# Optimization experiments

Measured on AMD Instinct MI355X. Metric: run time of the kernel, lower is better.

## Reference

```python
import jax, jax.numpy as jnp
import numpy as np

NEAR_LIDAR = 0.01
FAR_LIDAR = 0.81
BOUND = 1.0
DENSITY_SCALE = 1.0


def setup_inputs() -> dict:
    key = jax.random.key(0)
    ks = jax.random.split(key, 8)
    N = 8192
    H, F, OUT = 32, 16, 2
    return {
        "rays_o": jax.random.normal(ks[0], (1, N, 3), jnp.float32) * 0.1,
        "rays_d": jax.random.normal(ks[1], (1, N, 3), jnp.float32),
        "time": jax.random.uniform(ks[2], (1,), jnp.float32),
        "W1": jax.random.normal(ks[3], (4, H), jnp.float32) * 0.1,
        "b1": jnp.zeros((H,), jnp.float32),
        "Wsig": jax.random.normal(ks[4], (H, 1), jnp.float32) * 0.1,
        "Wfeat": jax.random.normal(ks[5], (H, F), jnp.float32) * 0.1,
        "Wa1": jax.random.normal(ks[6], (3 + 3 + F, H), jnp.float32) * 0.1,
        "ba1": jnp.zeros((H,), jnp.float32),
        "Wa2": jax.random.normal(ks[7], (H, OUT), jnp.float32) * 0.1,
        "num_steps": 512,
    }


def reference(rays_o, rays_d, time, W1, b1, Wsig, Wfeat, Wa1, ba1, Wa2, num_steps):
    prefix = rays_o.shape[:-1]
    ro = rays_o.reshape(-1, 3)
    rd = rays_d.reshape(-1, 3)
    N = ro.shape[0]
    dt = ro.dtype

    nears = jnp.full((N, 1), NEAR_LIDAR, dt)
    fars = jnp.full((N, 1), FAR_LIDAR, dt)
    z = jnp.linspace(0.0, 1.0, num_steps, dtype=dt)[None, :]  # [1,S]
    z_vals = nears + (fars - nears) * z                        # [N,S]
    sample_dist = (fars - nears) / num_steps                   # [N,1]

    # sample points, clamped to aabb [-bound, bound]
    xyzs = ro[:, None, :] + rd[:, None, :] * z_vals[..., None]  # [N,S,3]
    xyzs = jnp.clip(xyzs, -BOUND, BOUND)

    # density stub: MLP on (xyz, t) -> sigma, geo_feat
    t = jnp.broadcast_to(time.reshape(-1)[0].astype(dt), (N, num_steps, 1))
    h = jax.nn.relu(jnp.concatenate([xyzs, t], -1) @ W1 + b1)  # [N,S,H]
    sigma = jax.nn.softplus(h @ Wsig)[..., 0]                  # [N,S]
    feat = h @ Wfeat                                           # [N,S,F]

    deltas = z_vals[..., 1:] - z_vals[..., :-1]
    deltas = jnp.concatenate([deltas, jnp.broadcast_to(sample_dist, (N, 1))], -1)
    alphas = 1.0 - jnp.exp(-deltas * DENSITY_SCALE * sigma)    # [N,S]
    alphas_shifted = jnp.concatenate(
        [jnp.ones_like(alphas[..., :1]), 1.0 - alphas + 1e-15], -1)
    weights = alphas * jnp.cumprod(alphas_shifted, -1)[..., :-1]  # [N,S]

    # attribute stub: MLP on (xyz, dir, geo_feat) -> out_lidar_dim, sigmoid
    dirs = jnp.broadcast_to(rd[:, None, :], xyzs.shape)
    attr = jax.nn.sigmoid(
        jax.nn.relu(jnp.concatenate([xyzs, dirs, feat], -1) @ Wa1 + ba1) @ Wa2)

    weights_sum = weights.sum(-1)
    depth = (weights * z_vals).sum(-1)
    image = (weights[..., None] * attr).sum(-2)

    depth = depth.reshape(*prefix)
    image = image.reshape(*prefix, attr.shape[-1])
    weights_sum = weights_sum.reshape(*prefix)
    return depth, image, weights_sum
```

## Files before the change

kernel.cpp:

```cpp
#include <hip/hip_runtime.h>
#include <math.h>

typedef unsigned short u16;
typedef unsigned int   u32;
typedef unsigned long long u64;

typedef __attribute__((ext_vector_type(8))) short     short8;
typedef __attribute__((ext_vector_type(8))) _Float16  half8;
typedef __attribute__((ext_vector_type(2))) __fp16    fp16x2;
typedef __attribute__((ext_vector_type(4))) float     f32x4;
typedef __attribute__((ext_vector_type(2))) float     f32x2;

__device__ __forceinline__ float bf2f(u16 u){ return __uint_as_float(((u32)u)<<16); }
__device__ __forceinline__ u16 f2bf(float f){ u32 x=__float_as_uint(f); return (u16)((x + 0x7FFFu + ((x>>16)&1u))>>16); }
__device__ __forceinline__ u16 f2h_bits(float x){ union{_Float16 f; u16 u;} c; c.f=(_Float16)x; return c.u; }
__device__ __forceinline__ float h2f(u16 b){ union{u16 u; _Float16 f;} c; c.u=b; return (float)c.f; }
__device__ __forceinline__ u32 pkrtz2(float a, float b){
    union{fp16x2 h; u32 u;} c; c.h = __builtin_amdgcn_cvt_pkrtz(a,b); return c.u;
}
__device__ __forceinline__ u32 pk_relu(float a, float b){
    u32 pk = pkrtz2(a, b), r;
    asm("v_pk_max_f16 %0, %1, 0" : "=v"(r) : "v"(pk));
    return r;
}
__device__ __forceinline__ float clamp1(float x){ return __builtin_amdgcn_fmed3f(x, -1.f, 1.f); }
__device__ __forceinline__ float sigmoidf_fast(float x){ return __builtin_amdgcn_rcpf(1.f + __expf(-x)); }
__device__ __forceinline__ float softplusf_fast(float x){ return (x > 15.f) ? x : __logf(1.f + __expf(x)); }
__device__ __forceinline__ void lds_fence(){ asm volatile("s_waitcnt lgkmcnt(0)" ::: "memory"); }

__device__ __forceinline__ int sniff_is_bf16(const void* rays_d) {
    const u16* p = (const u16*)rays_d;
    int sane = 0;
    #pragma unroll
    for (int k = 0; k < 32; ++k) {
        u16 u = p[2 * k];
        int e = (u >> 7) & 0xFF;
        if (u == 0 || (e >= 96 && e <= 144)) ++sane;
    }
    return sane >= 24;
}
__device__ __forceinline__ float ldin(const void* base, int idx, int isbf) {
    return isbf ? bf2f(((const u16*)base)[idx]) : ((const float*)base)[idx];
}

#define NEARL 0.01f
#define FARL  0.81f

__device__ __forceinline__ int unitof(int k){ return (k>>1) + 16*(k&1); }

__global__ void prep_weights(const void* __restrict__ rays_d,
                             const void* __restrict__ W1,  const void* __restrict__ b1,
                             const void* __restrict__ Wsig,const void* __restrict__ Wfeat,
                             const void* __restrict__ Wa1, const void* __restrict__ ba1,
                             const void* __restrict__ Wa2, u16* __restrict__ wsb)
{
    __shared__ float raw[1504];
    const int tid = threadIdx.x;
    const int isbf = sniff_is_bf16(rays_d);
    for (int i = tid; i < 1504; i += 512) {
        float v;
        if (i < 128)       v = ldin(W1,   i,        isbf);
        else if (i < 160)  v = ldin(b1,   i - 128,  isbf);
        else if (i < 192)  v = ldin(Wsig, i - 160,  isbf);
        else if (i < 704)  v = ldin(Wfeat,i - 192,  isbf);
        else if (i < 1408) v = ldin(Wa1,  i - 704,  isbf);
        else if (i < 1440) v = ldin(ba1,  i - 1408, isbf);
        else               v = ldin(Wa2,  i - 1440, isbf);
        raw[i] = v;
    }
    __syncthreads();
    const float* rW1  = raw;
    const float* rb1  = raw + 128;
    const float* rWs  = raw + 160;
    const float* rWf  = raw + 192;
    const float* rWa1 = raw + 704;
    const float* rba  = raw + 1408;
    const float* rWa2 = raw + 1440;

    const int p = tid >> 6, l = tid & 63;
    const int q = l >> 4, n = l & 15;
    for (int j = 0; j < 8; ++j) {
        const int k = q * 8 + j;
        float v = 0.f;
        if (p == 0 || p == 1) {
            const int nn = n + 16 * p;
            if (k < 4)       v = rW1[k * 32 + nn];
            else if (k == 4) v = rb1[nn];
        } else if (p == 2) {
            if (n == 0) v = rWs[unitof(k)];
        } else if (p == 3 || p == 4) {
            const int nn = n + 16 * (p - 3);
            const int u = unitof(k);
            float acc = 0.f;
            for (int f = 0; f < 16; ++f)
                acc += rWf[u * 16 + f] * rWa1[(6 + f) * 32 + nn];
            v = acc;
        } else if (p == 5 || p == 6) {
            const int nn = n + 16 * (p - 5);
            if (k < 6)       v = rWa1[k * 32 + nn];
            else if (k == 6) v = rba[nn];
        } else {
            if (n < 2) v = rWa2[unitof(k) * 2 + n];
        }
        wsb[p * 512 + l * 8 + j] = f2h_bits(v);
    }
}

#define MFMA(a,b,c) __builtin_amdgcn_mfma_f32_16x16x32_f16((a),(b),(c),0,0,0)

union FA { half8 h; short8 s; u32 u[4]; };

__global__ __launch_bounds__(256, 4)
void lidar_fwd(const void* __restrict__ rays_o, const void* __restrict__ rays_d,
               const void* __restrict__ timep, const int* __restrict__ nstep,
               const u16* __restrict__ wsb, void* __restrict__ out, int N)
{
    __shared__ u16   hs [4][16][44];
    __shared__ float sigs[4][512];
    __shared__ u16   at0s[4][512];
    __shared__ u16   at1s[4][512];

    const int lane = threadIdx.x & 63;
    const int w    = threadIdx.x >> 6;
    const int ray  = blockIdx.x * 4 + w;
    if (ray >= N) return;

    const int q = lane >> 4;
    const int c = lane & 15;

    const int isbf = sniff_is_bf16(rays_d);
    const int S  = nstep[0];
    const int TL = S >> 4;

    const float tf = ldin(timep, 0, isbf);
    const float ox = ldin(rays_o, ray*3+0, isbf);
    const float oy = ldin(rays_o, ray*3+1, isbf);
    const float oz = ldin(rays_o, ray*3+2, isbf);
    const float rx = ldin(rays_d, ray*3+0, isbf);
    const float ry = ldin(rays_d, ray*3+1, isbf);
    const float rz = ldin(rays_d, ray*3+2, isbf);

    const float span  = FARL - NEARL;
    const float inv   = 1.f / (float)(S - 1);
    const float dzv   = span * inv;
    const float dlast = span / (float)S;

    const short8* bp = (const short8*)wsb;
    FA B1a, B1b, Bs, Bca, Bcb, Bxa, Bxb, Ba;
    B1a.s = bp[0*64+lane]; B1b.s = bp[1*64+lane];
    Bs.s  = bp[2*64+lane];
    Bca.s = bp[3*64+lane]; Bcb.s = bp[4*64+lane];
    Bxa.s = bp[5*64+lane]; Bxb.s = bp[6*64+lane];
    Ba.s  = bp[7*64+lane];

    const u32 pk_dydz = pkrtz2(ry, rz);
    const f32x4 z4 = {0.f, 0.f, 0.f, 0.f};

    for (int tl = 0; tl < TL; ++tl) {
        const int s0 = tl * 16;
        const float zz = NEARL + span * ((float)(s0 + c) * inv);
        const float ax = clamp1(ox + rx * zz);
        const float ay = clamp1(oy + ry * zz);
        const float az = clamp1(oz + rz * zz);
        const u32 pkxy = pkrtz2(ax, ay);

        FA A1;
        A1.u[0] = (q == 0) ? pkxy : 0u;
        A1.u[1] = (q == 0) ? pkrtz2(az, tf) : 0u;
        A1.u[2] = (q == 0) ? 0x00003C00u : 0u;
        A1.u[3] = 0u;
        FA A7;
        A7.u[0] = A1.u[0];
        A7.u[1] = (q == 0) ? pkrtz2(az, rx) : 0u;
        A7.u[2] = (q == 0) ? pk_dydz : 0u;
        A7.u[3] = (q == 0) ? 0x00003C00u : 0u;

        f32x4 c0 = MFMA(A1.h, B1a.h, z4);
        f32x4 c1 = MFMA(A1.h, B1b.h, z4);
        f32x4 e0 = MFMA(A7.h, Bxa.h, z4);
        f32x4 e1 = MFMA(A7.h, Bxb.h, z4);

        #pragma unroll
        for (int r = 0; r < 4; ++r)
            *(u32*)&hs[w][q*4 + r][2*c] = pk_relu(c0[r], c1[r]);
        lds_fence();

        FA Ah; Ah.s = *(const short8*)&hs[w][c][q*8];
        f32x4 cs = MFMA(Ah.h, Bs.h, z4);
        f32x4 d0 = MFMA(Ah.h, Bca.h, e0);
        f32x4 d1 = MFMA(Ah.h, Bcb.h, e1);
        if (c == 0)
            *(f32x4*)&sigs[w][s0 + q*4] = cs;

        #pragma unroll
        for (int r = 0; r < 4; ++r)
            *(u32*)&hs[w][q*4 + r][2*c] = pk_relu(d0[r], d1[r]);
        lds_fence();

        FA Ah2; Ah2.s = *(const short8*)&hs[w][c][q*8];
        f32x4 ca = MFMA(Ah2.h, Ba.h, z4);
        if (c < 2) {
            u64 pk = (u64)pkrtz2(ca[0], ca[1]) | ((u64)pkrtz2(ca[2], ca[3]) << 32);
            u16* d = (c == 0) ? &at0s[w][0] : &at1s[w][0];
            *(u64*)&d[s0 + q*4] = pk;
        }
    }
    lds_fence();

    const int P  = S >> 6;
    const int i0 = lane * P;
    const f32x4 sg0 = *(const f32x4*)&sigs[w][i0];
    const f32x4 sg1 = *(const f32x4*)&sigs[w][i0 + 4];
    const short8 a0v = *(const short8*)&at0s[w][i0];
    const short8 a1v = *(const short8*)&at1s[w][i0];

    float Trun = 1.f, Sw = 0.f, Sd = 0.f, Si0 = 0.f, Si1 = 0.f;
    #pragma unroll
    for (int j = 0; j < 8; ++j) {
        const int i = i0 + j;
        const float zz    = NEARL + span * ((float)i * inv);
        const float sigma = softplusf_fast(j < 4 ? sg0[j & 3] : sg1[j & 3]);
        const float dd    = (i == S - 1) ? dlast : dzv;
        const float e     = __expf(-dd * sigma);
        const float a     = 1.f - e;
        const float at0   = sigmoidf_fast(h2f((u16)a0v[j]));
        const float at1   = sigmoidf_fast(h2f((u16)a1v[j]));
        const float ww    = a * Trun;
        Sw += ww; Sd += ww * zz; Si0 += ww * at0; Si1 += ww * at1;
        Trun *= e + 1e-15f;
    }

    float T = Trun;
    #pragma unroll
    for (int off = 1; off < 64; off <<= 1) {
        float v = __shfl_up(T, off);
        if (lane >= off) T *= v;
    }
    float Texcl = __shfl_up(T, 1);
    if (lane == 0) Texcl = 1.f;
    Sw *= Texcl; Sd *= Texcl; Si0 *= Texcl; Si1 *= Texcl;

    #pragma unroll
    for (int off = 32; off > 0; off >>= 1) {
        Sw  += __shfl_down(Sw, off);
        Sd  += __shfl_down(Sd, off);
        Si0 += __shfl_down(Si0, off);
        Si1 += __shfl_down(Si1, off);
    }

    if (lane == 0) {
        if (isbf) {
            u16* o = (u16*)out;
            o[ray]             = f2bf(Sd);
            o[N + ray*2 + 0]   = f2bf(Si0);
            o[N + ray*2 + 1]   = f2bf(Si1);
            o[3*N + ray]       = f2bf(Sw);
        } else {
            float* o = (float*)out;
            o[ray]             = Sd;
            o[N + ray*2 + 0]   = Si0;
            o[N + ray*2 + 1]   = Si1;
            o[3*N + ray]       = Sw;
        }
    }
}

extern "C" void kernel_launch(void* const* d_in, const int* in_sizes, int n_in,
                              void* d_out, int out_size, void* d_ws, size_t ws_size,
                              hipStream_t stream) {
    const int N = in_sizes[0] / 3;
    u16* wsb = (u16*)d_ws;

    prep_weights<<<1, 512, 0, stream>>>(
        d_in[1], d_in[3], d_in[4], d_in[5],
        d_in[6], d_in[7], d_in[8], d_in[9], wsb);

    dim3 grid((N + 3) / 4);
    lidar_fwd<<<grid, 256, 0, stream>>>(
        d_in[0], d_in[1], d_in[2],
        (const int*)d_in[10], wsb, d_out, N);
}
```

Before: 128.1 us.

## Transpose MFMA chain so hidden activations stay in registers, skipping LDS round-trips

After: 116.5 us. 1.1x faster.

```diff
diff --git a/kernel.cpp b/kernel.cpp
--- a/kernel.cpp
+++ b/kernel.cpp
@@ -9,7 +9,7 @@
 typedef __attribute__((ext_vector_type(8))) _Float16  half8;
 typedef __attribute__((ext_vector_type(2))) __fp16    fp16x2;
 typedef __attribute__((ext_vector_type(4))) float     f32x4;
-typedef __attribute__((ext_vector_type(2))) float     f32x2;
+typedef __attribute__((ext_vector_type(4))) u32       u32x4;
 
 __device__ __forceinline__ float bf2f(u16 u){ return __uint_as_float(((u32)u)<<16); }
 __device__ __forceinline__ u16 f2bf(float f){ u32 x=__float_as_uint(f); return (u16)((x + 0x7FFFu + ((x>>16)&1u))>>16); }
@@ -46,13 +46,13 @@
 #define NEARL 0.01f
 #define FARL  0.81f
 
-__device__ __forceinline__ int unitof(int k){ return (k>>1) + 16*(k&1); }
+__device__ __forceinline__ int sigk(int q, int j){ return ((j >> 2) << 4) + q * 4 + (j & 3); }
 
 __global__ void prep_weights(const void* __restrict__ rays_d,
                              const void* __restrict__ W1,  const void* __restrict__ b1,
                              const void* __restrict__ Wsig,const void* __restrict__ Wfeat,
                              const void* __restrict__ Wa1, const void* __restrict__ ba1,
-                             const void* __restrict__ Wa2, u16* __restrict__ wsb)
+                             const void* __restrict__ Wa2, u16* __restrict__ wsa)
 {
     __shared__ float raw[1504];
     const int tid = threadIdx.x;
@@ -78,31 +78,30 @@
     const float* rWa2 = raw + 1440;
 
     const int p = tid >> 6, l = tid & 63;
-    const int q = l >> 4, n = l & 15;
+    const int m = l & 15, q = l >> 4;
     for (int j = 0; j < 8; ++j) {
-        const int k = q * 8 + j;
         float v = 0.f;
         if (p == 0 || p == 1) {
-            const int nn = n + 16 * p;
-            if (k < 4)       v = rW1[k * 32 + nn];
-            else if (k == 4) v = rb1[nn];
-        } else if (p == 2) {
-            if (n == 0) v = rWs[unitof(k)];
-        } else if (p == 3 || p == 4) {
-            const int nn = n + 16 * (p - 3);
-            const int u = unitof(k);
+            const int mm = m + 16 * p;
+            if (j < 4)       v = rW1[j * 32 + mm];
+            else if (j == 4) v = rb1[mm];
+        } else if (p == 2 || p == 3) {
+            const int mm = m + 16 * (p - 2);
+            if (j < 6)       v = rWa1[j * 32 + mm];
+            else if (j == 6) v = rba[mm];
+        } else if (p == 4 || p == 5) {
+            const int mm = m + 16 * (p - 4);
+            const int u = sigk(q, j);
             float acc = 0.f;
             for (int f = 0; f < 16; ++f)
-                acc += rWf[u * 16 + f] * rWa1[(6 + f) * 32 + nn];
+                acc += rWf[u * 16 + f] * rWa1[(6 + f) * 32 + mm];
             v = acc;
-        } else if (p == 5 || p == 6) {
-            const int nn = n + 16 * (p - 5);
-            if (k < 6)       v = rWa1[k * 32 + nn];
-            else if (k == 6) v = rba[nn];
+        } else if (p == 6) {
+            if (m == 0) v = rWs[sigk(q, j)];
         } else {
-            if (n < 2) v = rWa2[unitof(k) * 2 + n];
+            if (m < 2) v = rWa2[sigk(q, j) * 2 + m];
         }
-        wsb[p * 512 + l * 8 + j] = f2h_bits(v);
+        wsa[p * 512 + l * 8 + j] = f2h_bits(v);
     }
 }
 
@@ -113,12 +112,10 @@
 __global__ __launch_bounds__(256, 4)
 void lidar_fwd(const void* __restrict__ rays_o, const void* __restrict__ rays_d,
                const void* __restrict__ timep, const int* __restrict__ nstep,
-               const u16* __restrict__ wsb, void* __restrict__ out, int N)
+               const u16* __restrict__ wsa, void* __restrict__ out, int N)
 {
-    __shared__ u16   hs [4][16][44];
     __shared__ float sigs[4][512];
-    __shared__ u16   at0s[4][512];
-    __shared__ u16   at1s[4][512];
+    __shared__ u32   at01[4][512];
 
     const int lane = threadIdx.x & 63;
     const int w    = threadIdx.x >> 6;
@@ -145,13 +142,12 @@
     const float dzv   = span * inv;
     const float dlast = span / (float)S;
 
-    const short8* bp = (const short8*)wsb;
-    FA B1a, B1b, Bs, Bca, Bcb, Bxa, Bxb, Ba;
-    B1a.s = bp[0*64+lane]; B1b.s = bp[1*64+lane];
-    Bs.s  = bp[2*64+lane];
-    Bca.s = bp[3*64+lane]; Bcb.s = bp[4*64+lane];
-    Bxa.s = bp[5*64+lane]; Bxb.s = bp[6*64+lane];
-    Ba.s  = bp[7*64+lane];
+    const short8* bp = (const short8*)wsa;
+    FA P0, P1, Px0, Px1, Pc0, Pc1, Ps, Pa;
+    P0.s  = bp[0*64+lane]; P1.s  = bp[1*64+lane];
+    Px0.s = bp[2*64+lane]; Px1.s = bp[3*64+lane];
+    Pc0.s = bp[4*64+lane]; Pc1.s = bp[5*64+lane];
+    Ps.s  = bp[6*64+lane]; Pa.s  = bp[7*64+lane];
 
     const u32 pk_dydz = pkrtz2(ry, rz);
     const f32x4 z4 = {0.f, 0.f, 0.f, 0.f};
@@ -164,55 +160,48 @@
         const float az = clamp1(oz + rz * zz);
         const u32 pkxy = pkrtz2(ax, ay);
 
-        FA A1;
-        A1.u[0] = (q == 0) ? pkxy : 0u;
-        A1.u[1] = (q == 0) ? pkrtz2(az, tf) : 0u;
-        A1.u[2] = (q == 0) ? 0x00003C00u : 0u;
-        A1.u[3] = 0u;
-        FA A7;
-        A7.u[0] = A1.u[0];
-        A7.u[1] = (q == 0) ? pkrtz2(az, rx) : 0u;
-        A7.u[2] = (q == 0) ? pk_dydz : 0u;
-        A7.u[3] = (q == 0) ? 0x00003C00u : 0u;
-
-        f32x4 c0 = MFMA(A1.h, B1a.h, z4);
-        f32x4 c1 = MFMA(A1.h, B1b.h, z4);
-        f32x4 e0 = MFMA(A7.h, Bxa.h, z4);
-        f32x4 e1 = MFMA(A7.h, Bxb.h, z4);
-
-        #pragma unroll
-        for (int r = 0; r < 4; ++r)
-            *(u32*)&hs[w][q*4 + r][2*c] = pk_relu(c0[r], c1[r]);
-        lds_fence();
-
-        FA Ah; Ah.s = *(const short8*)&hs[w][c][q*8];
-        f32x4 cs = MFMA(Ah.h, Bs.h, z4);
-        f32x4 d0 = MFMA(Ah.h, Bca.h, e0);
-        f32x4 d1 = MFMA(Ah.h, Bcb.h, e1);
-        if (c == 0)
-            *(f32x4*)&sigs[w][s0 + q*4] = cs;
-
-        #pragma unroll
-        for (int r = 0; r < 4; ++r)
-            *(u32*)&hs[w][q*4 + r][2*c] = pk_relu(d0[r], d1[r]);
-        lds_fence();
-
-        FA Ah2; Ah2.s = *(const short8*)&hs[w][c][q*8];
-        f32x4 ca = MFMA(Ah2.h, Ba.h, z4);
-        if (c < 2) {
-            u64 pk = (u64)pkrtz2(ca[0], ca[1]) | ((u64)pkrtz2(ca[2], ca[3]) << 32);
-            u16* d = (c == 0) ? &at0s[w][0] : &at1s[w][0];
-            *(u64*)&d[s0 + q*4] = pk;
+        FA B1;
+        B1.u[0] = (q == 0) ? pkxy : 0u;
+        B1.u[1] = (q == 0) ? pkrtz2(az, tf) : 0u;
+        B1.u[2] = (q == 0) ? 0x00003C00u : 0u;
+        B1.u[3] = 0u;
+        FA B7;
+        B7.u[0] = B1.u[0];
+        B7.u[1] = (q == 0) ? pkrtz2(az, rx) : 0u;
+        B7.u[2] = (q == 0) ? pk_dydz : 0u;
+        B7.u[3] = (q == 0) ? 0x00003C00u : 0u;
+
+        f32x4 c0 = MFMA(P0.h,  B1.h, z4);
+        f32x4 c1 = MFMA(P1.h,  B1.h, z4);
+        f32x4 e0 = MFMA(Px0.h, B7.h, z4);
+        f32x4 e1 = MFMA(Px1.h, B7.h, z4);
+
+        FA Bh;
+        Bh.u[0] = pk_relu(c0[0], c0[1]); Bh.u[1] = pk_relu(c0[2], c0[3]);
+        Bh.u[2] = pk_relu(c1[0], c1[1]); Bh.u[3] = pk_relu(c1[2], c1[3]);
+
+        f32x4 cs = MFMA(Ps.h,  Bh.h, z4);
+        f32x4 d0 = MFMA(Pc0.h, Bh.h, e0);
+        f32x4 d1 = MFMA(Pc1.h, Bh.h, e1);
+
+        FA Bg;
+        Bg.u[0] = pk_relu(d0[0], d0[1]); Bg.u[1] = pk_relu(d0[2], d0[3]);
+        Bg.u[2] = pk_relu(d1[0], d1[1]); Bg.u[3] = pk_relu(d1[2], d1[3]);
+
+        f32x4 ca = MFMA(Pa.h, Bg.h, z4);
+
+        if (lane < 16) {
+            sigs[w][s0 + c] = cs[0];
+            at01[w][s0 + c] = pkrtz2(ca[0], ca[1]);
         }
     }
     lds_fence();
 
-    const int P  = S >> 6;
-    const int i0 = lane * P;
+    const int i0 = lane * (S >> 6);
     const f32x4 sg0 = *(const f32x4*)&sigs[w][i0];
     const f32x4 sg1 = *(const f32x4*)&sigs[w][i0 + 4];
-    const short8 a0v = *(const short8*)&at0s[w][i0];
-    const short8 a1v = *(const short8*)&at1s[w][i0];
+    const u32x4 av0 = *(const u32x4*)&at01[w][i0];
+    const u32x4 av1 = *(const u32x4*)&at01[w][i0 + 4];
 
     float Trun = 1.f, Sw = 0.f, Sd = 0.f, Si0 = 0.f, Si1 = 0.f;
     #pragma unroll
@@ -220,11 +209,12 @@
         const int i = i0 + j;
         const float zz    = NEARL + span * ((float)i * inv);
         const float sigma = softplusf_fast(j < 4 ? sg0[j & 3] : sg1[j & 3]);
+        const u32   apk   = j < 4 ? av0[j & 3] : av1[j & 3];
         const float dd    = (i == S - 1) ? dlast : dzv;
         const float e     = __expf(-dd * sigma);
         const float a     = 1.f - e;
-        const float at0   = sigmoidf_fast(h2f((u16)a0v[j]));
-        const float at1   = sigmoidf_fast(h2f((u16)a1v[j]));
+        const float at0   = sigmoidf_fast(h2f((u16)apk));
+        const float at1   = sigmoidf_fast(h2f((u16)(apk >> 16)));
         const float ww    = a * Trun;
         Sw += ww; Sd += ww * zz; Si0 += ww * at0; Si1 += ww * at1;
         Trun *= e + 1e-15f;
@@ -269,14 +259,14 @@
                               void* d_out, int out_size, void* d_ws, size_t ws_size,
                               hipStream_t stream) {
     const int N = in_sizes[0] / 3;
-    u16* wsb = (u16*)d_ws;
+    u16* wsa = (u16*)d_ws;
 
     prep_weights<<<1, 512, 0, stream>>>(
         d_in[1], d_in[3], d_in[4], d_in[5],
-        d_in[6], d_in[7], d_in[8], d_in[9], wsb);
+        d_in[6], d_in[7], d_in[8], d_in[9], wsa);
 
     dim3 grid((N + 3) / 4);
     lidar_fwd<<<grid, 256, 0, stream>>>(
         d_in[0], d_in[1], d_in[2],
-        (const int*)d_in[10], wsb, d_out, N);
-}
+        (const int*)d_in[10], wsa, d_out, N);
+}
```
